# Kernel optimization log

Measured on AMD Instinct MI355X. Metric: run time of the kernel, lower is better.

The kernel has to match this reference:

```python
import jax, jax.numpy as jnp
from jax import lax
import numpy as np

NPOINTS = 1024
B, N, C = 32, 100000, 3


def setup_inputs() -> dict:
    key = jax.random.key(0)
    k1, k2 = jax.random.split(key)
    coord = jax.random.normal(k1, (B, N, C), dtype=jnp.float32)
    farthest_init = jax.random.randint(k2, (B,), 0, N, dtype=jnp.int64)
    return {"coord": coord, "farthest_init": farthest_init}


def reference(coord, farthest_init):
    # coord: (B, N, 3); farthest_init: (B,) seed indices.
    Bs, Ns, _ = coord.shape
    init_distance = jnp.full((Bs, Ns), 1e10, dtype=coord.dtype)

    def step(carry, _):
        distance, farthest = carry
        # gather current centroid per batch: (B, 1, 3)
        centroid = jnp.take_along_axis(coord, farthest[:, None, None], axis=1)
        dist = jnp.sum((coord - centroid) ** 2, axis=-1)  # (B, N)
        distance = jnp.minimum(distance, dist)            # masked update
        new_farthest = jnp.argmax(distance, axis=-1)      # (B,)
        # record the index that was just used as centroid (pre-update), as in torch loop
        return (distance, new_farthest), farthest

    (_, _), centroids_t = lax.scan(step, (init_distance, farthest_init), None, length=NPOINTS)
    centroids = centroids_t.T  # (B, NPOINTS)
    # gather sampled coordinates: (B, NPOINTS, 3)
    sampled = jnp.take_along_axis(coord, centroids[:, :, None], axis=1)
    return centroids, sampled
```

## Files before the change

### kernel.cpp

```cpp
#include <hip/hip_runtime.h>
#include <stdint.h>

#define BATCHES 32
#define NPT     100000
#define NSAMP   1024
#define GPB     16
#define NPAIR   16
#define TPB     1024
#define NCW     15
#define CTH     (NCW*64)
#define PPB     6250
#define PPT     7
#define TAILT   490

typedef unsigned long long u64;
typedef unsigned int u32;

#define WS_BYTES (2 * BATCHES * GPB * 4 * 8)

__device__ __forceinline__ void red_ki(u64& key, u32& idx, int off) {
    u64 ok = __shfl_xor(key, off, 64);
    u32 oi = __shfl_xor(idx, off, 64);
    if (ok > key || (ok == key && oi < idx)) { key = ok; idx = oi; }
}

__device__ __forceinline__ void red_step(u64& key, u32& idx, float& x, float& y, float& z, int off) {
    u64   ok = __shfl_xor(key, off, 64);
    u32   oi = __shfl_xor(idx, off, 64);
    float ox = __shfl_xor(x, off, 64);
    float oy = __shfl_xor(y, off, 64);
    float oz = __shfl_xor(z, off, 64);
    if (ok > key || (ok == key && oi < idx)) { key = ok; idx = oi; x = ox; y = oy; z = oz; }
}

__global__ void
__attribute__((amdgpu_flat_work_group_size(TPB, TPB), amdgpu_waves_per_eu(4, 4)))
fps_kernel(const float* __restrict__ coord,
           const int* __restrict__ seed_raw,
           float* __restrict__ out,
           u64* __restrict__ rec)
{
    const int tid  = threadIdx.x;
    const int lane = tid & 63;
    const int wid  = tid >> 6;
    const int p    = (int)blockIdx.x & (NPAIR - 1);
    const int g    = (int)blockIdx.x >> 4;
    const int base = g * PPB;
    const int bA = p, bB = p + NPAIR;

    __shared__ u64 winw[2][2][2];
    __shared__ u32 sbar[8];
    __shared__ u64   pkey[2][NCW];
    __shared__ u32   pidx[2][NCW];
    __shared__ float pxs[2][NCW], pys[2][NCW], pzs[2][NCW];

    if (tid < 8) { sbar[tid] = 0; ((u64*)winw)[tid] = 0ull; }
    __syncthreads();

    float* cent_out = out;
    float* samp_out = out + BATCHES * NSAMP;

    if (wid == NCW) {
        for (int t = 1; t < NSAMP; ++t) {
            #pragma unroll
            for (int xb = 0; xb < 2; ++xb) {
                const int batch = xb ? bB : bA;
                u64* slot = rec + ((size_t)((t & 1) * BATCHES + batch) * GPB) * 4;
                const u64 t2 = (u64)(((t >> 1) + 1) & 3);
                const bool mine = lane < 3 * GPB;
                u64* wp = slot + (mine ? ((lane / 3) * 4 + (lane % 3)) : 0);
                u64 w = 0;
                for (;;) {
                    bool ok = true;
                    if (mine) {
                        w = __hip_atomic_load(wp, __ATOMIC_RELAXED, __HIP_MEMORY_SCOPE_AGENT);
                        ok = (w >> 62) == t2;
                    }
                    if (__ballot(ok) == ~0ull) break;
                    __builtin_amdgcn_s_sleep(1);
                }
                const int li = lane & 15;
                u64 w0 = __shfl(w, 3 * li + 0, 64);
                u64 w1 = __shfl(w, 3 * li + 1, 64);
                u64 w2 = __shfl(w, 3 * li + 2, 64);
                u64 k3 = 0ull; u32 i3 = 0xFFFFFFFFu; float x3 = 0.f, y3 = 0.f, z3 = 0.f;
                if (lane < GPB) {
                    k3 = (w0 & 0x3FFFFFFFFFFFFFFFull) | (((w1 >> 60) & 3ull) << 62);
                    u32 xbt = (u32)(w1 >> 28);
                    u32 ybt = (u32)(((w1 & 0xFFFFFFFull) << 4) | ((w2 >> 58) & 0xFull));
                    u32 zbt = (u32)(w2 >> 26);
                    i3 = (u32)((w2 >> 9) & 0x1FFFFu);
                    x3 = __uint_as_float(xbt); y3 = __uint_as_float(ybt); z3 = __uint_as_float(zbt);
                }
                red_step(k3, i3, x3, y3, z3, 8); red_step(k3, i3, x3, y3, z3, 4);
                red_step(k3, i3, x3, y3, z3, 2); red_step(k3, i3, x3, y3, z3, 1);
                if (lane == 0) {
                    u32 xbt = __float_as_uint(x3), ybt = __float_as_uint(y3), zbt = __float_as_uint(z3);
                    u64 v0 = (t2 << 62) | ((u64)xbt << 30) | (u64)(ybt >> 2);
                    u64 v1 = (t2 << 62) | ((u64)(ybt & 3u) << 60) | ((u64)zbt << 28) | ((u64)i3 << 11);
                    __hip_atomic_store(&winw[xb][t & 1][0], v0, __ATOMIC_RELAXED, __HIP_MEMORY_SCOPE_WORKGROUP);
                    __hip_atomic_store(&winw[xb][t & 1][1], v1, __ATOMIC_RELAXED, __HIP_MEMORY_SCOPE_WORKGROUP);
                }
            }
        }
        return;
    }

    const int ct = tid;
    const float* cbA = coord + (size_t)bA * (NPT * 3);
    const float* cbB = coord + (size_t)bB * (NPT * 3);

    int odd = 0;
    #pragma unroll
    for (int i = 1; i < 32; i += 2) odd |= seed_raw[i];
    u32 scur[2]; float scx[2], scy[2], scz[2];
    scur[0] = (u32)((odd == 0) ? seed_raw[2 * bA] : seed_raw[bA]);
    scur[1] = (u32)((odd == 0) ? seed_raw[2 * bB] : seed_raw[bB]);
    scx[0] = cbA[(size_t)scur[0] * 3 + 0]; scy[0] = cbA[(size_t)scur[0] * 3 + 1]; scz[0] = cbA[(size_t)scur[0] * 3 + 2];
    scx[1] = cbB[(size_t)scur[1] * 3 + 0]; scy[1] = cbB[(size_t)scur[1] * 3 + 1]; scz[1] = cbB[(size_t)scur[1] * 3 + 2];

    float  px[2][PPT], py[2][PPT], pz[2][PPT];
    double d[2][PPT];
    #pragma unroll
    for (int xb = 0; xb < 2; ++xb) {
        const float* cb = xb ? cbB : cbA;
        #pragma unroll
        for (int k = 0; k < PPT; ++k) {
            bool v = (k < PPT - 1) || (ct < TAILT);
            int gi = base + (v ? (k * CTH + ct) : 0);
            px[xb][k] = v ? cb[(size_t)gi * 3 + 0] : 0.f;
            py[xb][k] = v ? cb[(size_t)gi * 3 + 1] : 0.f;
            pz[xb][k] = v ? cb[(size_t)gi * 3 + 2] : 0.f;
            d[xb][k]  = v ? 1.0e10 : 0.0;
        }
    }

    for (int t = 0; t < NSAMP; ++t) {
        #pragma unroll
        for (int xb = 0; xb < 2; ++xb) {
            const int batch = xb ? bB : bA;
            const int pi = 2 * t + xb;
            u32 cur; float cx, cy, cz;
            if (t == 0) {
                cur = scur[xb]; cx = scx[xb]; cy = scy[xb]; cz = scz[xb];
            } else {
                const u64 t2 = (u64)(((t >> 1) + 1) & 3);
                u64 v0, v1;
                for (;;) {
                    v0 = __hip_atomic_load(&winw[xb][t & 1][0], __ATOMIC_RELAXED, __HIP_MEMORY_SCOPE_WORKGROUP);
                    v1 = __hip_atomic_load(&winw[xb][t & 1][1], __ATOMIC_RELAXED, __HIP_MEMORY_SCOPE_WORKGROUP);
                    if (((v0 >> 62) == t2) & ((v1 >> 62) == t2)) break;
                }
                u32 xbt = (u32)(v0 >> 30);
                u32 ybt = (u32)(((v0 & 0x3FFFFFFFull) << 2) | ((v1 >> 60) & 3ull));
                u32 zbt = (u32)(v1 >> 28);
                cur = (u32)((v1 >> 11) & 0x1FFFFu);
                cx = __uint_as_float(xbt); cy = __uint_as_float(ybt); cz = __uint_as_float(zbt);
            }
            if (g == 0 && wid == 1 && lane == 0) {
                cent_out[batch * NSAMP + t] = (float)cur;
                size_t so = ((size_t)batch * NSAMP + t) * 3;
                samp_out[so + 0] = cx; samp_out[so + 1] = cy; samp_out[so + 2] = cz;
            }
            if (t == NSAMP - 1) continue;

            const double cxd = (double)cx, cyd = (double)cy, czd = (double)cz;
            double bd = -1.0; u32 bi = 0; float bx = 0.f, by = 0.f, bz = 0.f;
            #pragma unroll
            for (int k = 0; k < PPT; ++k) {
                if (k == PPT - 1 && ct >= TAILT) break;
                double dx = __dsub_rn((double)px[xb][k], cxd);
                double dy = __dsub_rn((double)py[xb][k], cyd);
                double dz = __dsub_rn((double)pz[xb][k], czd);
                double d2 = __dadd_rn(__dadd_rn(__dmul_rn(dx, dx), __dmul_rn(dy, dy)),
                                      __dmul_rn(dz, dz));
                double nd = fmin(d[xb][k], d2);
                d[xb][k] = nd;
                bool gt = nd > bd;
                bd = gt ? nd : bd;
                bi = gt ? (u32)(base + k * CTH + ct) : bi;
                bx = gt ? px[xb][k] : bx;
                by = gt ? py[xb][k] : by;
                bz = gt ? pz[xb][k] : bz;
            }
            u64 key = (u64)__double_as_longlong(bd);

            u64 wk = key; u32 wi = bi;
            red_ki(wk, wi, 32); red_ki(wk, wi, 16); red_ki(wk, wi, 8);
            red_ki(wk, wi, 4);  red_ki(wk, wi, 2);  red_ki(wk, wi, 1);
            const int pb = pi & 1;
            if (wi == bi) { pkey[pb][wid] = wk; pidx[pb][wid] = wi;
                            pxs[pb][wid] = bx; pys[pb][wid] = by; pzs[pb][wid] = bz; }

            if (lane == 0)
                __hip_atomic_fetch_add(&sbar[pi & 7], 1u, __ATOMIC_RELEASE, __HIP_MEMORY_SCOPE_WORKGROUP);
            const u32 tgt = (u32)(NCW * ((pi >> 3) + 1));
            while (__hip_atomic_load(&sbar[pi & 7], __ATOMIC_ACQUIRE, __HIP_MEMORY_SCOPE_WORKGROUP) < tgt) {}

            if (wid == 0) {
                u64   k2 = (lane < NCW) ? pkey[pb][lane] : 0ull;
                u32   i2 = (lane < NCW) ? pidx[pb][lane] : 0xFFFFFFFFu;
                float x2 = (lane < NCW) ? pxs[pb][lane] : 0.f;
                float y2 = (lane < NCW) ? pys[pb][lane] : 0.f;
                float z2 = (lane < NCW) ? pzs[pb][lane] : 0.f;
                red_step(k2, i2, x2, y2, z2, 8); red_step(k2, i2, x2, y2, z2, 4);
                red_step(k2, i2, x2, y2, z2, 2); red_step(k2, i2, x2, y2, z2, 1);
                if (lane == 0) {
                    const u32 v = (u32)(t + 1);
                    const u64 t2p = (u64)(((v >> 1) + 1) & 3);
                    u64* r = rec + ((size_t)((v & 1) * BATCHES + batch) * GPB + g) * 4;
                    u32 xbt = __float_as_uint(x2), ybt = __float_as_uint(y2), zbt = __float_as_uint(z2);
                    u64 w0 = (t2p << 62) | (k2 & 0x3FFFFFFFFFFFFFFFull);
                    u64 w1 = (t2p << 62) | ((k2 >> 62) << 60) | ((u64)xbt << 28) | (u64)(ybt >> 4);
                    u64 w2 = (t2p << 62) | ((u64)(ybt & 0xFu) << 58) | ((u64)zbt << 26) | ((u64)i2 << 9);
                    __hip_atomic_store(&r[0], w0, __ATOMIC_RELAXED, __HIP_MEMORY_SCOPE_AGENT);
                    __hip_atomic_store(&r[1], w1, __ATOMIC_RELAXED, __HIP_MEMORY_SCOPE_AGENT);
                    __hip_atomic_store(&r[2], w2, __ATOMIC_RELAXED, __HIP_MEMORY_SCOPE_AGENT);
                }
            }
        }
    }
}

extern "C" void kernel_launch(void* const* d_in, const int* in_sizes, int n_in,
                              void* d_out, int out_size, void* d_ws, size_t ws_size,
                              hipStream_t stream)
{
    const float* coord = (const float*)d_in[0];
    const int*   seed  = (const int*)d_in[1];
    float* out = (float*)d_out;
    u64* rec = (u64*)d_ws;

    hipMemsetAsync(d_ws, 0, WS_BYTES, stream);
    fps_kernel<<<dim3(NPAIR * GPB), dim3(TPB), 0, stream>>>(coord, seed, out, rec);
}
```

Measured before the change: 4.373 ms.

## Split workgroup waves per batch with dedicated cross-block reducer waves

Instead of each compute wave processing both batches of the pair in sequence, the block now assigns 7 waves to each batch (14 points per thread), and two reducer waves each handle one batch. The intra-block barrier is split per batch, and only the leader wave waits on it, so the two batches' pipelines run independently and overlap. The global poll loop also drops s_sleep and keeps several loads in flight to cut handoff latency. The trade-offs are doubled per-thread register state, fewer waves sharing each batch's work, and busier spinning on memory.

```diff
diff --git a/kernel.cpp b/kernel.cpp
--- a/kernel.cpp
+++ b/kernel.cpp
@@ -7,11 +7,12 @@
 #define GPB     16
 #define NPAIR   16
 #define TPB     1024
-#define NCW     15
-#define CTH     (NCW*64)
+#define NCWAVES 14
+#define NCWB    7
+#define CTHB    (NCWB*64)
 #define PPB     6250
-#define PPT     7
-#define TAILT   490
+#define PPT     14
+#define TAILT   426
 
 typedef unsigned long long u64;
 typedef unsigned int u32;
@@ -49,174 +50,165 @@
     const int bA = p, bB = p + NPAIR;
 
     __shared__ u64 winw[2][2][2];
-    __shared__ u32 sbar[8];
-    __shared__ u64   pkey[2][NCW];
-    __shared__ u32   pidx[2][NCW];
-    __shared__ float pxs[2][NCW], pys[2][NCW], pzs[2][NCW];
-
-    if (tid < 8) { sbar[tid] = 0; ((u64*)winw)[tid] = 0ull; }
+    __shared__ u32 sbar[2][8];
+    __shared__ u64   pkey[2][2][NCWB];
+    __shared__ u32   pidx[2][2][NCWB];
+    __shared__ float pxs[2][2][NCWB], pys[2][2][NCWB], pzs[2][2][NCWB];
+
+    if (tid < 16) ((u32*)sbar)[tid] = 0u;
+    if (tid < 8)  ((u64*)winw)[tid] = 0ull;
     __syncthreads();
 
     float* cent_out = out;
     float* samp_out = out + BATCHES * NSAMP;
 
-    if (wid == NCW) {
+    if (wid >= NCWAVES) {
+        const int xb    = wid - NCWAVES;
+        const int batch = xb ? bB : bA;
+        const bool mine = lane < 3 * GPB;
+        const int  widx = mine ? ((lane / 3) * 4 + (lane % 3)) : 0;
         for (int t = 1; t < NSAMP; ++t) {
-            #pragma unroll
-            for (int xb = 0; xb < 2; ++xb) {
-                const int batch = xb ? bB : bA;
-                u64* slot = rec + ((size_t)((t & 1) * BATCHES + batch) * GPB) * 4;
-                const u64 t2 = (u64)(((t >> 1) + 1) & 3);
-                const bool mine = lane < 3 * GPB;
-                u64* wp = slot + (mine ? ((lane / 3) * 4 + (lane % 3)) : 0);
-                u64 w = 0;
-                for (;;) {
-                    bool ok = true;
-                    if (mine) {
-                        w = __hip_atomic_load(wp, __ATOMIC_RELAXED, __HIP_MEMORY_SCOPE_AGENT);
-                        ok = (w >> 62) == t2;
-                    }
-                    if (__ballot(ok) == ~0ull) break;
-                    __builtin_amdgcn_s_sleep(1);
-                }
-                const int li = lane & 15;
-                u64 w0 = __shfl(w, 3 * li + 0, 64);
-                u64 w1 = __shfl(w, 3 * li + 1, 64);
-                u64 w2 = __shfl(w, 3 * li + 2, 64);
-                u64 k3 = 0ull; u32 i3 = 0xFFFFFFFFu; float x3 = 0.f, y3 = 0.f, z3 = 0.f;
-                if (lane < GPB) {
-                    k3 = (w0 & 0x3FFFFFFFFFFFFFFFull) | (((w1 >> 60) & 3ull) << 62);
-                    u32 xbt = (u32)(w1 >> 28);
-                    u32 ybt = (u32)(((w1 & 0xFFFFFFFull) << 4) | ((w2 >> 58) & 0xFull));
-                    u32 zbt = (u32)(w2 >> 26);
-                    i3 = (u32)((w2 >> 9) & 0x1FFFFu);
-                    x3 = __uint_as_float(xbt); y3 = __uint_as_float(ybt); z3 = __uint_as_float(zbt);
-                }
-                red_step(k3, i3, x3, y3, z3, 8); red_step(k3, i3, x3, y3, z3, 4);
-                red_step(k3, i3, x3, y3, z3, 2); red_step(k3, i3, x3, y3, z3, 1);
-                if (lane == 0) {
-                    u32 xbt = __float_as_uint(x3), ybt = __float_as_uint(y3), zbt = __float_as_uint(z3);
-                    u64 v0 = (t2 << 62) | ((u64)xbt << 30) | (u64)(ybt >> 2);
-                    u64 v1 = (t2 << 62) | ((u64)(ybt & 3u) << 60) | ((u64)zbt << 28) | ((u64)i3 << 11);
-                    __hip_atomic_store(&winw[xb][t & 1][0], v0, __ATOMIC_RELAXED, __HIP_MEMORY_SCOPE_WORKGROUP);
-                    __hip_atomic_store(&winw[xb][t & 1][1], v1, __ATOMIC_RELAXED, __HIP_MEMORY_SCOPE_WORKGROUP);
-                }
+            u64* slot = rec + ((size_t)((t & 1) * BATCHES + batch) * GPB) * 4;
+            u64* wp   = slot + widx;
+            const u64 t2 = (u64)(((t >> 1) + 1) & 3);
+            u64 wa = __hip_atomic_load(wp, __ATOMIC_RELAXED, __HIP_MEMORY_SCOPE_AGENT);
+            u64 wb = __hip_atomic_load(wp, __ATOMIC_RELAXED, __HIP_MEMORY_SCOPE_AGENT);
+            u64 w;
+            for (;;) {
+                u64 wc = __hip_atomic_load(wp, __ATOMIC_RELAXED, __HIP_MEMORY_SCOPE_AGENT);
+                if (__ballot((!mine) || ((wa >> 62) == t2)) == ~0ull) { w = wa; break; }
+                wa = wb; wb = wc;
+            }
+            const int li = lane & 15;
+            u64 w0 = __shfl(w, 3 * li + 0, 64);
+            u64 w1 = __shfl(w, 3 * li + 1, 64);
+            u64 w2 = __shfl(w, 3 * li + 2, 64);
+            u64 k3 = 0ull; u32 i3 = 0xFFFFFFFFu; float x3 = 0.f, y3 = 0.f, z3 = 0.f;
+            if (lane < GPB) {
+                k3 = (w0 & 0x3FFFFFFFFFFFFFFFull) | (((w1 >> 60) & 3ull) << 62);
+                u32 xbt = (u32)(w1 >> 28);
+                u32 ybt = (u32)(((w1 & 0xFFFFFFFull) << 4) | ((w2 >> 58) & 0xFull));
+                u32 zbt = (u32)(w2 >> 26);
+                i3 = (u32)((w2 >> 9) & 0x1FFFFu);
+                x3 = __uint_as_float(xbt); y3 = __uint_as_float(ybt); z3 = __uint_as_float(zbt);
+            }
+            red_step(k3, i3, x3, y3, z3, 8); red_step(k3, i3, x3, y3, z3, 4);
+            red_step(k3, i3, x3, y3, z3, 2); red_step(k3, i3, x3, y3, z3, 1);
+            if (lane == 0) {
+                u32 xbt = __float_as_uint(x3), ybt = __float_as_uint(y3), zbt = __float_as_uint(z3);
+                u64 v0 = (t2 << 62) | ((u64)xbt << 30) | (u64)(ybt >> 2);
+                u64 v1 = (t2 << 62) | ((u64)(ybt & 3u) << 60) | ((u64)zbt << 28) | ((u64)i3 << 11);
+                __hip_atomic_store(&winw[xb][t & 1][0], v0, __ATOMIC_RELAXED, __HIP_MEMORY_SCOPE_WORKGROUP);
+                __hip_atomic_store(&winw[xb][t & 1][1], v1, __ATOMIC_RELAXED, __HIP_MEMORY_SCOPE_WORKGROUP);
             }
         }
         return;
     }
 
-    const int ct = tid;
-    const float* cbA = coord + (size_t)bA * (NPT * 3);
-    const float* cbB = coord + (size_t)bB * (NPT * 3);
+    const int xb    = (wid >= NCWB) ? 1 : 0;
+    const int wid7  = wid - xb * NCWB;
+    const int ct    = tid - xb * CTHB;
+    const int batch = xb ? bB : bA;
+    const float* cb = coord + (size_t)batch * (NPT * 3);
 
     int odd = 0;
     #pragma unroll
     for (int i = 1; i < 32; i += 2) odd |= seed_raw[i];
-    u32 scur[2]; float scx[2], scy[2], scz[2];
-    scur[0] = (u32)((odd == 0) ? seed_raw[2 * bA] : seed_raw[bA]);
-    scur[1] = (u32)((odd == 0) ? seed_raw[2 * bB] : seed_raw[bB]);
-    scx[0] = cbA[(size_t)scur[0] * 3 + 0]; scy[0] = cbA[(size_t)scur[0] * 3 + 1]; scz[0] = cbA[(size_t)scur[0] * 3 + 2];
-    scx[1] = cbB[(size_t)scur[1] * 3 + 0]; scy[1] = cbB[(size_t)scur[1] * 3 + 1]; scz[1] = cbB[(size_t)scur[1] * 3 + 2];
-
-    float  px[2][PPT], py[2][PPT], pz[2][PPT];
-    double d[2][PPT];
+    u32 scur = (u32)((odd == 0) ? seed_raw[2 * batch] : seed_raw[batch]);
+    float scx = cb[(size_t)scur * 3 + 0];
+    float scy = cb[(size_t)scur * 3 + 1];
+    float scz = cb[(size_t)scur * 3 + 2];
+
+    float  px[PPT], py[PPT], pz[PPT];
+    double d[PPT];
     #pragma unroll
-    for (int xb = 0; xb < 2; ++xb) {
-        const float* cb = xb ? cbB : cbA;
+    for (int k = 0; k < PPT; ++k) {
+        bool v = (k < PPT - 1) || (ct < TAILT);
+        int gi = base + (v ? (k * CTHB + ct) : 0);
+        px[k] = v ? cb[(size_t)gi * 3 + 0] : 0.f;
+        py[k] = v ? cb[(size_t)gi * 3 + 1] : 0.f;
+        pz[k] = v ? cb[(size_t)gi * 3 + 2] : 0.f;
+        d[k]  = v ? 1.0e10 : 0.0;
+    }
+
+    for (int t = 0; t < NSAMP; ++t) {
+        u32 cur; float cx, cy, cz;
+        if (t == 0) {
+            cur = scur; cx = scx; cy = scy; cz = scz;
+        } else {
+            const u64 t2 = (u64)(((t >> 1) + 1) & 3);
+            u64 v0, v1;
+            for (;;) {
+                v0 = __hip_atomic_load(&winw[xb][t & 1][0], __ATOMIC_RELAXED, __HIP_MEMORY_SCOPE_WORKGROUP);
+                v1 = __hip_atomic_load(&winw[xb][t & 1][1], __ATOMIC_RELAXED, __HIP_MEMORY_SCOPE_WORKGROUP);
+                if (((v0 >> 62) == t2) & ((v1 >> 62) == t2)) break;
+            }
+            u32 xbt = (u32)(v0 >> 30);
+            u32 ybt = (u32)(((v0 & 0x3FFFFFFFull) << 2) | ((v1 >> 60) & 3ull));
+            u32 zbt = (u32)(v1 >> 28);
+            cur = (u32)((v1 >> 11) & 0x1FFFFu);
+            cx = __uint_as_float(xbt); cy = __uint_as_float(ybt); cz = __uint_as_float(zbt);
+        }
+        if (g == 0 && wid7 == 1 && lane == 0) {
+            cent_out[batch * NSAMP + t] = (float)cur;
+            size_t so = ((size_t)batch * NSAMP + t) * 3;
+            samp_out[so + 0] = cx; samp_out[so + 1] = cy; samp_out[so + 2] = cz;
+        }
+        if (t == NSAMP - 1) continue;
+
+        const double cxd = (double)cx, cyd = (double)cy, czd = (double)cz;
+        double bd = -1.0; u32 bi = 0; float bx = 0.f, by = 0.f, bz = 0.f;
         #pragma unroll
         for (int k = 0; k < PPT; ++k) {
-            bool v = (k < PPT - 1) || (ct < TAILT);
-            int gi = base + (v ? (k * CTH + ct) : 0);
-            px[xb][k] = v ? cb[(size_t)gi * 3 + 0] : 0.f;
-            py[xb][k] = v ? cb[(size_t)gi * 3 + 1] : 0.f;
-            pz[xb][k] = v ? cb[(size_t)gi * 3 + 2] : 0.f;
-            d[xb][k]  = v ? 1.0e10 : 0.0;
-        }
-    }
-
-    for (int t = 0; t < NSAMP; ++t) {
-        #pragma unroll
-        for (int xb = 0; xb < 2; ++xb) {
-            const int batch = xb ? bB : bA;
-            const int pi = 2 * t + xb;
-            u32 cur; float cx, cy, cz;
-            if (t == 0) {
-                cur = scur[xb]; cx = scx[xb]; cy = scy[xb]; cz = scz[xb];
-            } else {
-                const u64 t2 = (u64)(((t >> 1) + 1) & 3);
-                u64 v0, v1;
-                for (;;) {
-                    v0 = __hip_atomic_load(&winw[xb][t & 1][0], __ATOMIC_RELAXED, __HIP_MEMORY_SCOPE_WORKGROUP);
-                    v1 = __hip_atomic_load(&winw[xb][t & 1][1], __ATOMIC_RELAXED, __HIP_MEMORY_SCOPE_WORKGROUP);
-                    if (((v0 >> 62) == t2) & ((v1 >> 62) == t2)) break;
-                }
-                u32 xbt = (u32)(v0 >> 30);
-                u32 ybt = (u32)(((v0 & 0x3FFFFFFFull) << 2) | ((v1 >> 60) & 3ull));
-                u32 zbt = (u32)(v1 >> 28);
-                cur = (u32)((v1 >> 11) & 0x1FFFFu);
-                cx = __uint_as_float(xbt); cy = __uint_as_float(ybt); cz = __uint_as_float(zbt);
-            }
-            if (g == 0 && wid == 1 && lane == 0) {
-                cent_out[batch * NSAMP + t] = (float)cur;
-                size_t so = ((size_t)batch * NSAMP + t) * 3;
-                samp_out[so + 0] = cx; samp_out[so + 1] = cy; samp_out[so + 2] = cz;
-            }
-            if (t == NSAMP - 1) continue;
-
-            const double cxd = (double)cx, cyd = (double)cy, czd = (double)cz;
-            double bd = -1.0; u32 bi = 0; float bx = 0.f, by = 0.f, bz = 0.f;
-            #pragma unroll
-            for (int k = 0; k < PPT; ++k) {
-                if (k == PPT - 1 && ct >= TAILT) break;
-                double dx = __dsub_rn((double)px[xb][k], cxd);
-                double dy = __dsub_rn((double)py[xb][k], cyd);
-                double dz = __dsub_rn((double)pz[xb][k], czd);
-                double d2 = __dadd_rn(__dadd_rn(__dmul_rn(dx, dx), __dmul_rn(dy, dy)),
-                                      __dmul_rn(dz, dz));
-                double nd = fmin(d[xb][k], d2);
-                d[xb][k] = nd;
-                bool gt = nd > bd;
-                bd = gt ? nd : bd;
-                bi = gt ? (u32)(base + k * CTH + ct) : bi;
-                bx = gt ? px[xb][k] : bx;
-                by = gt ? py[xb][k] : by;
-                bz = gt ? pz[xb][k] : bz;
-            }
-            u64 key = (u64)__double_as_longlong(bd);
-
-            u64 wk = key; u32 wi = bi;
-            red_ki(wk, wi, 32); red_ki(wk, wi, 16); red_ki(wk, wi, 8);
-            red_ki(wk, wi, 4);  red_ki(wk, wi, 2);  red_ki(wk, wi, 1);
-            const int pb = pi & 1;
-            if (wi == bi) { pkey[pb][wid] = wk; pidx[pb][wid] = wi;
-                            pxs[pb][wid] = bx; pys[pb][wid] = by; pzs[pb][wid] = bz; }
-
-            if (lane == 0)
-                __hip_atomic_fetch_add(&sbar[pi & 7], 1u, __ATOMIC_RELEASE, __HIP_MEMORY_SCOPE_WORKGROUP);
-            const u32 tgt = (u32)(NCW * ((pi >> 3) + 1));
-            while (__hip_atomic_load(&sbar[pi & 7], __ATOMIC_ACQUIRE, __HIP_MEMORY_SCOPE_WORKGROUP) < tgt) {}
-
-            if (wid == 0) {
-                u64   k2 = (lane < NCW) ? pkey[pb][lane] : 0ull;
-                u32   i2 = (lane < NCW) ? pidx[pb][lane] : 0xFFFFFFFFu;
-                float x2 = (lane < NCW) ? pxs[pb][lane] : 0.f;
-                float y2 = (lane < NCW) ? pys[pb][lane] : 0.f;
-                float z2 = (lane < NCW) ? pzs[pb][lane] : 0.f;
-                red_step(k2, i2, x2, y2, z2, 8); red_step(k2, i2, x2, y2, z2, 4);
-                red_step(k2, i2, x2, y2, z2, 2); red_step(k2, i2, x2, y2, z2, 1);
-                if (lane == 0) {
-                    const u32 v = (u32)(t + 1);
-                    const u64 t2p = (u64)(((v >> 1) + 1) & 3);
-                    u64* r = rec + ((size_t)((v & 1) * BATCHES + batch) * GPB + g) * 4;
-                    u32 xbt = __float_as_uint(x2), ybt = __float_as_uint(y2), zbt = __float_as_uint(z2);
-                    u64 w0 = (t2p << 62) | (k2 & 0x3FFFFFFFFFFFFFFFull);
-                    u64 w1 = (t2p << 62) | ((k2 >> 62) << 60) | ((u64)xbt << 28) | (u64)(ybt >> 4);
-                    u64 w2 = (t2p << 62) | ((u64)(ybt & 0xFu) << 58) | ((u64)zbt << 26) | ((u64)i2 << 9);
-                    __hip_atomic_store(&r[0], w0, __ATOMIC_RELAXED, __HIP_MEMORY_SCOPE_AGENT);
-                    __hip_atomic_store(&r[1], w1, __ATOMIC_RELAXED, __HIP_MEMORY_SCOPE_AGENT);
-                    __hip_atomic_store(&r[2], w2, __ATOMIC_RELAXED, __HIP_MEMORY_SCOPE_AGENT);
-                }
+            if (k == PPT - 1 && ct >= TAILT) break;
+            double dx = __dsub_rn((double)px[k], cxd);
+            double dy = __dsub_rn((double)py[k], cyd);
+            double dz = __dsub_rn((double)pz[k], czd);
+            double d2 = __dadd_rn(__dadd_rn(__dmul_rn(dx, dx), __dmul_rn(dy, dy)),
+                                  __dmul_rn(dz, dz));
+            double nd = fmin(d[k], d2);
+            d[k] = nd;
+            bool gt = nd > bd;
+            bd = gt ? nd : bd;
+            bi = gt ? (u32)(base + k * CTHB + ct) : bi;
+            bx = gt ? px[k] : bx;
+            by = gt ? py[k] : by;
+            bz = gt ? pz[k] : bz;
+        }
+        u64 key = (u64)__double_as_longlong(bd);
+
+        u64 wk = key; u32 wi = bi;
+        red_ki(wk, wi, 32); red_ki(wk, wi, 16); red_ki(wk, wi, 8);
+        red_ki(wk, wi, 4);  red_ki(wk, wi, 2);  red_ki(wk, wi, 1);
+        const int pb = t & 1;
+        if (wi == bi) { pkey[xb][pb][wid7] = wk; pidx[xb][pb][wid7] = wi;
+                        pxs[xb][pb][wid7] = bx; pys[xb][pb][wid7] = by; pzs[xb][pb][wid7] = bz; }
+
+        if (lane == 0)
+            __hip_atomic_fetch_add(&sbar[xb][t & 7], 1u, __ATOMIC_RELEASE, __HIP_MEMORY_SCOPE_WORKGROUP);
+
+        if (wid7 == 0) {
+            const u32 tgt = (u32)(NCWB * ((t >> 3) + 1));
+            while (__hip_atomic_load(&sbar[xb][t & 7], __ATOMIC_ACQUIRE, __HIP_MEMORY_SCOPE_WORKGROUP) < tgt) {}
+
+            u64   k2 = (lane < NCWB) ? pkey[xb][pb][lane] : 0ull;
+            u32   i2 = (lane < NCWB) ? pidx[xb][pb][lane] : 0xFFFFFFFFu;
+            float x2 = (lane < NCWB) ? pxs[xb][pb][lane] : 0.f;
+            float y2 = (lane < NCWB) ? pys[xb][pb][lane] : 0.f;
+            float z2 = (lane < NCWB) ? pzs[xb][pb][lane] : 0.f;
+            red_step(k2, i2, x2, y2, z2, 4); red_step(k2, i2, x2, y2, z2, 2);
+            red_step(k2, i2, x2, y2, z2, 1);
+            if (lane == 0) {
+                const u32 v = (u32)(t + 1);
+                const u64 t2p = (u64)(((v >> 1) + 1) & 3);
+                u64* r = rec + ((size_t)((v & 1) * BATCHES + batch) * GPB + g) * 4;
+                u32 xbt = __float_as_uint(x2), ybt = __float_as_uint(y2), zbt = __float_as_uint(z2);
+                u64 w0 = (t2p << 62) | (k2 & 0x3FFFFFFFFFFFFFFFull);
+                u64 w1 = (t2p << 62) | ((k2 >> 62) << 60) | ((u64)xbt << 28) | (u64)(ybt >> 4);
+                u64 w2 = (t2p << 62) | ((u64)(ybt & 0xFu) << 58) | ((u64)zbt << 26) | ((u64)i2 << 9);
+                __hip_atomic_store(&r[0], w0, __ATOMIC_RELAXED, __HIP_MEMORY_SCOPE_AGENT);
+                __hip_atomic_store(&r[1], w1, __ATOMIC_RELAXED, __HIP_MEMORY_SCOPE_AGENT);
+                __hip_atomic_store(&r[2], w2, __ATOMIC_RELAXED, __HIP_MEMORY_SCOPE_AGENT);
             }
         }
     }
```

After: 6.783 ms. 1.55x slower.

## Interleave four batches per block across 32 groups with per-batch reducer waves

Applied to the files above, without the earlier changes.

Each block now handles four batches instead of two, and each batch is split across 32 blocks instead of 16, so every thread holds fewer points (4 instead of 7 per batch). The total block count stays the same. Three collector waves now merge the 32 per-group records, with a wider shuffle-based record decode. The intra-block barrier wait is limited to one designated wave per batch, so the other compute waves can move straight on to the next batch without spinning. The aim is to hide the cross-block synchronization latency by interleaving four independent batches. The cost is more inter-block record traffic and polling per step, and with only 13 compute waves the sbar counter indexing must stay consistent.

```diff
diff --git a/kernel.cpp b/kernel.cpp
--- a/kernel.cpp
+++ b/kernel.cpp
@@ -4,14 +4,15 @@
 #define BATCHES 32
 #define NPT     100000
 #define NSAMP   1024
-#define GPB     16
-#define NPAIR   16
+#define NBAT    4
+#define NQUAD   8
+#define GPB     32
 #define TPB     1024
-#define NCW     15
+#define NCW     13
 #define CTH     (NCW*64)
-#define PPB     6250
-#define PPT     7
-#define TAILT   490
+#define PPB     3125
+#define PPT     4
+#define TAILT   629
 
 typedef unsigned long long u64;
 typedef unsigned int u32;
@@ -43,48 +44,48 @@
     const int tid  = threadIdx.x;
     const int lane = tid & 63;
     const int wid  = tid >> 6;
-    const int p    = (int)blockIdx.x & (NPAIR - 1);
-    const int g    = (int)blockIdx.x >> 4;
+    const int q    = (int)blockIdx.x & (NQUAD - 1);
+    const int g    = (int)blockIdx.x >> 3;
     const int base = g * PPB;
-    const int bA = p, bB = p + NPAIR;
-
-    __shared__ u64 winw[2][2][2];
+
+    __shared__ u64 winw[NBAT][2][2];
     __shared__ u32 sbar[8];
-    __shared__ u64   pkey[2][NCW];
-    __shared__ u32   pidx[2][NCW];
-    __shared__ float pxs[2][NCW], pys[2][NCW], pzs[2][NCW];
-
-    if (tid < 8) { sbar[tid] = 0; ((u64*)winw)[tid] = 0ull; }
+    __shared__ u64   pkey[NBAT][NCW];
+    __shared__ u32   pidx[NBAT][NCW];
+    __shared__ float pxs[NBAT][NCW], pys[NBAT][NCW], pzs[NBAT][NCW];
+
+    if (tid < 8)  sbar[tid] = 0u;
+    if (tid < 16) ((u64*)winw)[tid] = 0ull;
     __syncthreads();
 
     float* cent_out = out;
     float* samp_out = out + BATCHES * NSAMP;
 
-    if (wid == NCW) {
+    if (wid >= NCW) {
+        const int sw = wid - NCW;
+        const int x0 = (sw < 2) ? sw : 2;
+        const int nx = (sw < 2) ? 1 : 2;
+        const int gA = lane & 31;
         for (int t = 1; t < NSAMP; ++t) {
-            #pragma unroll
-            for (int xb = 0; xb < 2; ++xb) {
-                const int batch = xb ? bB : bA;
+            const u64 t2 = (u64)(((t >> 1) + 1) & 3);
+            for (int xi = 0; xi < nx; ++xi) {
+                const int xb = x0 + xi;
+                const int batch = q + NQUAD * xb;
                 u64* slot = rec + ((size_t)((t & 1) * BATCHES + batch) * GPB) * 4;
-                const u64 t2 = (u64)(((t >> 1) + 1) & 3);
-                const bool mine = lane < 3 * GPB;
-                u64* wp = slot + (mine ? ((lane / 3) * 4 + (lane % 3)) : 0);
-                u64 w = 0;
+                u64* wpP = slot + gA * 4 + ((lane >> 5) & 1);
+                u64* wpS = slot + gA * 4 + 2;
+                u64 vp, vs;
                 for (;;) {
-                    bool ok = true;
-                    if (mine) {
-                        w = __hip_atomic_load(wp, __ATOMIC_RELAXED, __HIP_MEMORY_SCOPE_AGENT);
-                        ok = (w >> 62) == t2;
-                    }
+                    vp = __hip_atomic_load(wpP, __ATOMIC_RELAXED, __HIP_MEMORY_SCOPE_AGENT);
+                    vs = __hip_atomic_load(wpS, __ATOMIC_RELAXED, __HIP_MEMORY_SCOPE_AGENT);
+                    bool ok = ((vp >> 62) == t2) & (((vs >> 62) == t2) | (lane >= 32));
                     if (__ballot(ok) == ~0ull) break;
                     __builtin_amdgcn_s_sleep(1);
                 }
-                const int li = lane & 15;
-                u64 w0 = __shfl(w, 3 * li + 0, 64);
-                u64 w1 = __shfl(w, 3 * li + 1, 64);
-                u64 w2 = __shfl(w, 3 * li + 2, 64);
+                u64 w1 = __shfl(vp, 32 + gA, 64);
                 u64 k3 = 0ull; u32 i3 = 0xFFFFFFFFu; float x3 = 0.f, y3 = 0.f, z3 = 0.f;
-                if (lane < GPB) {
+                if (lane < 32) {
+                    u64 w0 = vp, w2 = vs;
                     k3 = (w0 & 0x3FFFFFFFFFFFFFFFull) | (((w1 >> 60) & 3ull) << 62);
                     u32 xbt = (u32)(w1 >> 28);
                     u32 ybt = (u32)(((w1 & 0xFFFFFFFull) << 4) | ((w2 >> 58) & 0xFull));
@@ -92,8 +93,9 @@
                     i3 = (u32)((w2 >> 9) & 0x1FFFFu);
                     x3 = __uint_as_float(xbt); y3 = __uint_as_float(ybt); z3 = __uint_as_float(zbt);
                 }
-                red_step(k3, i3, x3, y3, z3, 8); red_step(k3, i3, x3, y3, z3, 4);
-                red_step(k3, i3, x3, y3, z3, 2); red_step(k3, i3, x3, y3, z3, 1);
+                red_step(k3, i3, x3, y3, z3, 16); red_step(k3, i3, x3, y3, z3, 8);
+                red_step(k3, i3, x3, y3, z3, 4);  red_step(k3, i3, x3, y3, z3, 2);
+                red_step(k3, i3, x3, y3, z3, 1);
                 if (lane == 0) {
                     u32 xbt = __float_as_uint(x3), ybt = __float_as_uint(y3), zbt = __float_as_uint(z3);
                     u64 v0 = (t2 << 62) | ((u64)xbt << 30) | (u64)(ybt >> 2);
@@ -107,23 +109,26 @@
     }
 
     const int ct = tid;
-    const float* cbA = coord + (size_t)bA * (NPT * 3);
-    const float* cbB = coord + (size_t)bB * (NPT * 3);
 
     int odd = 0;
     #pragma unroll
     for (int i = 1; i < 32; i += 2) odd |= seed_raw[i];
-    u32 scur[2]; float scx[2], scy[2], scz[2];
-    scur[0] = (u32)((odd == 0) ? seed_raw[2 * bA] : seed_raw[bA]);
-    scur[1] = (u32)((odd == 0) ? seed_raw[2 * bB] : seed_raw[bB]);
-    scx[0] = cbA[(size_t)scur[0] * 3 + 0]; scy[0] = cbA[(size_t)scur[0] * 3 + 1]; scz[0] = cbA[(size_t)scur[0] * 3 + 2];
-    scx[1] = cbB[(size_t)scur[1] * 3 + 0]; scy[1] = cbB[(size_t)scur[1] * 3 + 1]; scz[1] = cbB[(size_t)scur[1] * 3 + 2];
-
-    float  px[2][PPT], py[2][PPT], pz[2][PPT];
-    double d[2][PPT];
+    u32 scur[NBAT]; float scx[NBAT], scy[NBAT], scz[NBAT];
     #pragma unroll
-    for (int xb = 0; xb < 2; ++xb) {
-        const float* cb = xb ? cbB : cbA;
+    for (int xb = 0; xb < NBAT; ++xb) {
+        const int batch = q + NQUAD * xb;
+        const float* cb = coord + (size_t)batch * (NPT * 3);
+        scur[xb] = (u32)((odd == 0) ? seed_raw[2 * batch] : seed_raw[batch]);
+        scx[xb] = cb[(size_t)scur[xb] * 3 + 0];
+        scy[xb] = cb[(size_t)scur[xb] * 3 + 1];
+        scz[xb] = cb[(size_t)scur[xb] * 3 + 2];
+    }
+
+    float  px[NBAT][PPT], py[NBAT][PPT], pz[NBAT][PPT];
+    double d[NBAT][PPT];
+    #pragma unroll
+    for (int xb = 0; xb < NBAT; ++xb) {
+        const float* cb = coord + (size_t)(q + NQUAD * xb) * (NPT * 3);
         #pragma unroll
         for (int k = 0; k < PPT; ++k) {
             bool v = (k < PPT - 1) || (ct < TAILT);
@@ -137,9 +142,9 @@
 
     for (int t = 0; t < NSAMP; ++t) {
         #pragma unroll
-        for (int xb = 0; xb < 2; ++xb) {
-            const int batch = xb ? bB : bA;
-            const int pi = 2 * t + xb;
+        for (int xb = 0; xb < NBAT; ++xb) {
+            const int batch = q + NQUAD * xb;
+            const int pi = NBAT * t + xb;
             u32 cur; float cx, cy, cz;
             if (t == 0) {
                 cur = scur[xb]; cx = scx[xb]; cy = scy[xb]; cz = scz[xb];
@@ -188,21 +193,21 @@
             u64 wk = key; u32 wi = bi;
             red_ki(wk, wi, 32); red_ki(wk, wi, 16); red_ki(wk, wi, 8);
             red_ki(wk, wi, 4);  red_ki(wk, wi, 2);  red_ki(wk, wi, 1);
-            const int pb = pi & 1;
-            if (wi == bi) { pkey[pb][wid] = wk; pidx[pb][wid] = wi;
-                            pxs[pb][wid] = bx; pys[pb][wid] = by; pzs[pb][wid] = bz; }
+            if (wi == bi) { pkey[xb][wid] = wk; pidx[xb][wid] = wi;
+                            pxs[xb][wid] = bx; pys[xb][wid] = by; pzs[xb][wid] = bz; }
 
             if (lane == 0)
                 __hip_atomic_fetch_add(&sbar[pi & 7], 1u, __ATOMIC_RELEASE, __HIP_MEMORY_SCOPE_WORKGROUP);
-            const u32 tgt = (u32)(NCW * ((pi >> 3) + 1));
-            while (__hip_atomic_load(&sbar[pi & 7], __ATOMIC_ACQUIRE, __HIP_MEMORY_SCOPE_WORKGROUP) < tgt) {}
-
-            if (wid == 0) {
-                u64   k2 = (lane < NCW) ? pkey[pb][lane] : 0ull;
-                u32   i2 = (lane < NCW) ? pidx[pb][lane] : 0xFFFFFFFFu;
-                float x2 = (lane < NCW) ? pxs[pb][lane] : 0.f;
-                float y2 = (lane < NCW) ? pys[pb][lane] : 0.f;
-                float z2 = (lane < NCW) ? pzs[pb][lane] : 0.f;
+
+            if (wid == xb) {
+                const u32 tgt = (u32)(NCW * ((pi >> 3) + 1));
+                while (__hip_atomic_load(&sbar[pi & 7], __ATOMIC_ACQUIRE, __HIP_MEMORY_SCOPE_WORKGROUP) < tgt) {}
+
+                u64   k2 = (lane < NCW) ? pkey[xb][lane] : 0ull;
+                u32   i2 = (lane < NCW) ? pidx[xb][lane] : 0xFFFFFFFFu;
+                float x2 = (lane < NCW) ? pxs[xb][lane] : 0.f;
+                float y2 = (lane < NCW) ? pys[xb][lane] : 0.f;
+                float z2 = (lane < NCW) ? pzs[xb][lane] : 0.f;
                 red_step(k2, i2, x2, y2, z2, 8); red_step(k2, i2, x2, y2, z2, 4);
                 red_step(k2, i2, x2, y2, z2, 2); red_step(k2, i2, x2, y2, z2, 1);
                 if (lane == 0) {
@@ -232,5 +237,5 @@
     u64* rec = (u64*)d_ws;
 
     hipMemsetAsync(d_ws, 0, WS_BYTES, stream);
-    fps_kernel<<<dim3(NPAIR * GPB), dim3(TPB), 0, stream>>>(coord, seed, out, rec);
-}
+    fps_kernel<<<dim3(NQUAD * GPB), dim3(TPB), 0, stream>>>(coord, seed, out, rec);
+}
```

New measurement: 7.815 ms. 78.7% more time.

## Split global combiner per batch and rotate intra-block reducer wave without block-wide wait

Applied to the files above, without the earlier changes.

The single global-combiner wave that served both batches in turn becomes two waves, one per batch, so each batch's cross-block reduction can go on in parallel. This cuts the compute waves from 15 to 14 and adjusts the tail count to match. Within each step only one designated wave now waits on the shared counter and does the block-level reduction; that role rotates across waves each step, and the other waves skip the spin wait. The global poll loop now sleeps first and issues its next load before checking the previous value. In exchange, each remaining compute thread covers more points, and correctness relies on the inter-step dependency to keep the per-batch shared slots from being overwritten early.

```diff
diff --git a/kernel.cpp b/kernel.cpp
--- a/kernel.cpp
+++ b/kernel.cpp
@@ -7,11 +7,11 @@
 #define GPB     16
 #define NPAIR   16
 #define TPB     1024
-#define NCW     15
+#define NCW     14
 #define CTH     (NCW*64)
 #define PPB     6250
 #define PPT     7
-#define TAILT   490
+#define TAILT   874
 
 typedef unsigned long long u64;
 typedef unsigned int u32;
@@ -60,47 +60,45 @@
     float* cent_out = out;
     float* samp_out = out + BATCHES * NSAMP;
 
-    if (wid == NCW) {
+    if (wid >= NCW) {
+        const int xb    = wid - NCW;
+        const int batch = xb ? bB : bA;
+        const bool mine = lane < 3 * GPB;
+        const int  widx = mine ? ((lane / 3) * 4 + (lane % 3)) : 0;
         for (int t = 1; t < NSAMP; ++t) {
-            #pragma unroll
-            for (int xb = 0; xb < 2; ++xb) {
-                const int batch = xb ? bB : bA;
-                u64* slot = rec + ((size_t)((t & 1) * BATCHES + batch) * GPB) * 4;
-                const u64 t2 = (u64)(((t >> 1) + 1) & 3);
-                const bool mine = lane < 3 * GPB;
-                u64* wp = slot + (mine ? ((lane / 3) * 4 + (lane % 3)) : 0);
-                u64 w = 0;
-                for (;;) {
-                    bool ok = true;
-                    if (mine) {
-                        w = __hip_atomic_load(wp, __ATOMIC_RELAXED, __HIP_MEMORY_SCOPE_AGENT);
-                        ok = (w >> 62) == t2;
-                    }
-                    if (__ballot(ok) == ~0ull) break;
-                    __builtin_amdgcn_s_sleep(1);
-                }
-                const int li = lane & 15;
-                u64 w0 = __shfl(w, 3 * li + 0, 64);
-                u64 w1 = __shfl(w, 3 * li + 1, 64);
-                u64 w2 = __shfl(w, 3 * li + 2, 64);
-                u64 k3 = 0ull; u32 i3 = 0xFFFFFFFFu; float x3 = 0.f, y3 = 0.f, z3 = 0.f;
-                if (lane < GPB) {
-                    k3 = (w0 & 0x3FFFFFFFFFFFFFFFull) | (((w1 >> 60) & 3ull) << 62);
-                    u32 xbt = (u32)(w1 >> 28);
-                    u32 ybt = (u32)(((w1 & 0xFFFFFFFull) << 4) | ((w2 >> 58) & 0xFull));
-                    u32 zbt = (u32)(w2 >> 26);
-                    i3 = (u32)((w2 >> 9) & 0x1FFFFu);
-                    x3 = __uint_as_float(xbt); y3 = __uint_as_float(ybt); z3 = __uint_as_float(zbt);
-                }
-                red_step(k3, i3, x3, y3, z3, 8); red_step(k3, i3, x3, y3, z3, 4);
-                red_step(k3, i3, x3, y3, z3, 2); red_step(k3, i3, x3, y3, z3, 1);
-                if (lane == 0) {
-                    u32 xbt = __float_as_uint(x3), ybt = __float_as_uint(y3), zbt = __float_as_uint(z3);
-                    u64 v0 = (t2 << 62) | ((u64)xbt << 30) | (u64)(ybt >> 2);
-                    u64 v1 = (t2 << 62) | ((u64)(ybt & 3u) << 60) | ((u64)zbt << 28) | ((u64)i3 << 11);
-                    __hip_atomic_store(&winw[xb][t & 1][0], v0, __ATOMIC_RELAXED, __HIP_MEMORY_SCOPE_WORKGROUP);
-                    __hip_atomic_store(&winw[xb][t & 1][1], v1, __ATOMIC_RELAXED, __HIP_MEMORY_SCOPE_WORKGROUP);
-                }
+            u64* slot = rec + ((size_t)((t & 1) * BATCHES + batch) * GPB) * 4;
+            u64* wp   = slot + widx;
+            const u64 t2 = (u64)(((t >> 1) + 1) & 3);
+            u64 va = mine ? __hip_atomic_load(wp, __ATOMIC_RELAXED, __HIP_MEMORY_SCOPE_AGENT) : 0ull;
+            u64 w;
+            for (;;) {
+                __builtin_amdgcn_s_sleep(2);
+                u64 vb = mine ? __hip_atomic_load(wp, __ATOMIC_RELAXED, __HIP_MEMORY_SCOPE_AGENT) : 0ull;
+                bool ok = (!mine) || ((va >> 62) == t2);
+                if (__ballot(ok) == ~0ull) { w = va; break; }
+                va = vb;
+            }
+            const int li = lane & 15;
+            u64 w0 = __shfl(w, 3 * li + 0, 64);
+            u64 w1 = __shfl(w, 3 * li + 1, 64);
+            u64 w2 = __shfl(w, 3 * li + 2, 64);
+            u64 k3 = 0ull; u32 i3 = 0xFFFFFFFFu; float x3 = 0.f, y3 = 0.f, z3 = 0.f;
+            if (lane < GPB) {
+                k3 = (w0 & 0x3FFFFFFFFFFFFFFFull) | (((w1 >> 60) & 3ull) << 62);
+                u32 xbt = (u32)(w1 >> 28);
+                u32 ybt = (u32)(((w1 & 0xFFFFFFFull) << 4) | ((w2 >> 58) & 0xFull));
+                u32 zbt = (u32)(w2 >> 26);
+                i3 = (u32)((w2 >> 9) & 0x1FFFFu);
+                x3 = __uint_as_float(xbt); y3 = __uint_as_float(ybt); z3 = __uint_as_float(zbt);
+            }
+            red_step(k3, i3, x3, y3, z3, 8); red_step(k3, i3, x3, y3, z3, 4);
+            red_step(k3, i3, x3, y3, z3, 2); red_step(k3, i3, x3, y3, z3, 1);
+            if (lane == 0) {
+                u32 xbt = __float_as_uint(x3), ybt = __float_as_uint(y3), zbt = __float_as_uint(z3);
+                u64 v0 = (t2 << 62) | ((u64)xbt << 30) | (u64)(ybt >> 2);
+                u64 v1 = (t2 << 62) | ((u64)(ybt & 3u) << 60) | ((u64)zbt << 28) | ((u64)i3 << 11);
+                __hip_atomic_store(&winw[xb][t & 1][0], v0, __ATOMIC_RELAXED, __HIP_MEMORY_SCOPE_WORKGROUP);
+                __hip_atomic_store(&winw[xb][t & 1][1], v1, __ATOMIC_RELAXED, __HIP_MEMORY_SCOPE_WORKGROUP);
             }
         }
         return;
@@ -134,6 +132,8 @@
             d[xb][k]  = v ? 1.0e10 : 0.0;
         }
     }
+
+    int lr = 0;
 
     for (int t = 0; t < NSAMP; ++t) {
         #pragma unroll
@@ -157,7 +157,7 @@
                 cur = (u32)((v1 >> 11) & 0x1FFFFu);
                 cx = __uint_as_float(xbt); cy = __uint_as_float(ybt); cz = __uint_as_float(zbt);
             }
-            if (g == 0 && wid == 1 && lane == 0) {
+            if (g == 0 && wid == 2 && lane == 0) {
                 cent_out[batch * NSAMP + t] = (float)cur;
                 size_t so = ((size_t)batch * NSAMP + t) * 3;
                 samp_out[so + 0] = cx; samp_out[so + 1] = cy; samp_out[so + 2] = cz;
@@ -188,21 +188,21 @@
             u64 wk = key; u32 wi = bi;
             red_ki(wk, wi, 32); red_ki(wk, wi, 16); red_ki(wk, wi, 8);
             red_ki(wk, wi, 4);  red_ki(wk, wi, 2);  red_ki(wk, wi, 1);
-            const int pb = pi & 1;
-            if (wi == bi) { pkey[pb][wid] = wk; pidx[pb][wid] = wi;
-                            pxs[pb][wid] = bx; pys[pb][wid] = by; pzs[pb][wid] = bz; }
+            if (wi == bi) { pkey[xb][wid] = wk; pidx[xb][wid] = wi;
+                            pxs[xb][wid] = bx; pys[xb][wid] = by; pzs[xb][wid] = bz; }
 
             if (lane == 0)
                 __hip_atomic_fetch_add(&sbar[pi & 7], 1u, __ATOMIC_RELEASE, __HIP_MEMORY_SCOPE_WORKGROUP);
-            const u32 tgt = (u32)(NCW * ((pi >> 3) + 1));
-            while (__hip_atomic_load(&sbar[pi & 7], __ATOMIC_ACQUIRE, __HIP_MEMORY_SCOPE_WORKGROUP) < tgt) {}
-
-            if (wid == 0) {
-                u64   k2 = (lane < NCW) ? pkey[pb][lane] : 0ull;
-                u32   i2 = (lane < NCW) ? pidx[pb][lane] : 0xFFFFFFFFu;
-                float x2 = (lane < NCW) ? pxs[pb][lane] : 0.f;
-                float y2 = (lane < NCW) ? pys[pb][lane] : 0.f;
-                float z2 = (lane < NCW) ? pzs[pb][lane] : 0.f;
+
+            if (wid == lr + xb) {
+                const u32 tgt = (u32)(NCW * ((pi >> 3) + 1));
+                while (__hip_atomic_load(&sbar[pi & 7], __ATOMIC_ACQUIRE, __HIP_MEMORY_SCOPE_WORKGROUP) < tgt) {}
+
+                u64   k2 = (lane < NCW) ? pkey[xb][lane] : 0ull;
+                u32   i2 = (lane < NCW) ? pidx[xb][lane] : 0xFFFFFFFFu;
+                float x2 = (lane < NCW) ? pxs[xb][lane] : 0.f;
+                float y2 = (lane < NCW) ? pys[xb][lane] : 0.f;
+                float z2 = (lane < NCW) ? pzs[xb][lane] : 0.f;
                 red_step(k2, i2, x2, y2, z2, 8); red_step(k2, i2, x2, y2, z2, 4);
                 red_step(k2, i2, x2, y2, z2, 2); red_step(k2, i2, x2, y2, z2, 1);
                 if (lane == 0) {
@@ -219,6 +219,7 @@
                 }
             }
         }
+        lr += 2; if (lr == NCW) lr = 0;
     }
 }
 
```

Result: slower. 7.088 ms (+62.1%).
